# Performance work log

Measured on AMD Instinct MI355X. Metric: run time of the kernel, lower is better.

Reference implementation:

```python
import jax, jax.numpy as jnp
import numpy as np

D_MODEL = 1024
N_HEAD = 16
D_K = D_MODEL // N_HEAD
FFN = 4096
EPS = 1e-5


def layer_norm(x, g, b):
    mu = jnp.mean(x, axis=-1, keepdims=True)
    var = jnp.var(x, axis=-1, keepdims=True)
    return (x - mu) * jax.lax.rsqrt(var + EPS) * g + b


def setup_inputs() -> dict:
    key = jax.random.key(0)
    ks = jax.random.split(key, 16)
    B, L = 2, 2048
    s = 1.0 / np.sqrt(D_MODEL)
    inp = {
        "x": jax.random.normal(ks[0], (B, L, D_MODEL), dtype=jnp.float32),
        "mask": jnp.ones((B, 1, 1, L), dtype=jnp.int32),
        "ln1_g": jnp.ones((D_MODEL,), jnp.float32),
        "ln1_b": jnp.zeros((D_MODEL,), jnp.float32),
        "Wq": jax.random.normal(ks[1], (D_MODEL, D_MODEL), jnp.float32) * s,
        "bq": jnp.zeros((D_MODEL,), jnp.float32),
        "Wk": jax.random.normal(ks[2], (D_MODEL, D_MODEL), jnp.float32) * s,
        "bk": jnp.zeros((D_MODEL,), jnp.float32),
        "Wv": jax.random.normal(ks[3], (D_MODEL, D_MODEL), jnp.float32) * s,
        "bv": jnp.zeros((D_MODEL,), jnp.float32),
        "Wo": jax.random.normal(ks[4], (D_MODEL, D_MODEL), jnp.float32) * s,
        "bo": jnp.zeros((D_MODEL,), jnp.float32),
        "ln2_g": jnp.ones((D_MODEL,), jnp.float32),
        "ln2_b": jnp.zeros((D_MODEL,), jnp.float32),
        "W1": jax.random.normal(ks[5], (D_MODEL, FFN), jnp.float32) * s,
        "b1": jnp.zeros((FFN,), jnp.float32),
        "W2": jax.random.normal(ks[6], (FFN, D_MODEL), jnp.float32) * (1.0 / np.sqrt(FFN)),
        "b2": jnp.zeros((D_MODEL,), jnp.float32),
    }
    return inp


def reference(x, mask, ln1_g, ln1_b, Wq, bq, Wk, bk, Wv, bv, Wo, bo,
              ln2_g, ln2_b, W1, b1, W2, b2):
    B, L, _ = x.shape
    nx = layer_norm(x, ln1_g, ln1_b)
    # QKV projections, split heads -> [B, H, L, Dk]
    def proj(W, b):
        return (nx @ W + b).reshape(B, L, N_HEAD, D_K).transpose(0, 2, 1, 3)
    q, k, v = proj(Wq, bq), proj(Wk, bk), proj(Wv, bv)
    scores = jnp.einsum('bhqd,bhkd->bhqk', q, k) / np.sqrt(D_K)
    scores = jnp.where(mask.astype(bool), scores, -jnp.inf)
    attn = jax.nn.softmax(scores, axis=-1)
    out = jnp.einsum('bhqk,bhkd->bhqd', attn, v)
    out = out.transpose(0, 2, 1, 3).reshape(B, L, D_MODEL)
    out = out @ Wo + bo
    x = x + out  # residual (dropout p=0)
    nx = layer_norm(x, ln2_g, ln2_b)
    h = jax.nn.silu(nx @ W1 + b1)
    x = x + (h @ W2 + b2)
    return x
```

## Files before the change

kernel.cpp:

```cpp
#include <hip/hip_runtime.h>
#include <hip/hip_bf16.h>

#define D_MODEL 1024
#define N_HEAD  16
#define D_K     64
#define FFN_DIM 4096
#define B_SZ    2
#define L_SEQ   2048
#define ROWS    (B_SZ * L_SEQ)
#define PST     68

typedef float  floatx4 __attribute__((ext_vector_type(4)));
typedef short  shortx8 __attribute__((ext_vector_type(8)));

__device__ __forceinline__ unsigned short f2bf(float f) {
    unsigned int u = __float_as_uint(f);
    unsigned int rounding = 0x7fffu + ((u >> 16) & 1u);
    return (unsigned short)((u + rounding) >> 16);
}
__device__ __forceinline__ float bf2f(unsigned short u) {
    return __uint_as_float(((unsigned int)u) << 16);
}

__device__ __forceinline__ void glds16(const unsigned short* g, unsigned short* l) {
    __builtin_amdgcn_global_load_lds(
        (const __attribute__((address_space(1))) unsigned int*)g,
        (__attribute__((address_space(3))) unsigned int*)l, 16, 0, 0);
}

__device__ __forceinline__ void xcd_remap_gemm(int& bx, int& by, int& bz) {
    const int gx = gridDim.x, gy = gridDim.y, gz = gridDim.z;
    const int o = blockIdx.x + gx * (blockIdx.y + gy * blockIdx.z);
    const int nwg = gx * gy * gz;
    const int t = (o & 7) * (nwg >> 3) + (o >> 3);
    const int zsz = gx * gy;
    bz = t / zsz;
    const int w = t - bz * zsz;
    const int grp = w / (8 * gy);
    const int in  = w - grp * (8 * gy);
    by = in >> 3;
    bx = grp * 8 + (in & 7);
}

__global__ __launch_bounds__(256) void ln_kernel(const float* __restrict__ x,
                                                 const float* __restrict__ g,
                                                 const float* __restrict__ b,
                                                 unsigned short* __restrict__ out) {
    const int row = blockIdx.x;
    const int tid = threadIdx.x;
    const float* xr = x + (size_t)row * D_MODEL;
    float4 xv = *reinterpret_cast<const float4*>(&xr[tid * 4]);
    float v[4] = {xv.x, xv.y, xv.z, xv.w};
    float s = v[0] + v[1] + v[2] + v[3];
    float ss = v[0] * v[0] + v[1] * v[1] + v[2] * v[2] + v[3] * v[3];
    __shared__ float r1[256], r2[256];
    r1[tid] = s; r2[tid] = ss;
    __syncthreads();
    for (int off = 128; off > 0; off >>= 1) {
        if (tid < off) { r1[tid] += r1[tid + off]; r2[tid] += r2[tid + off]; }
        __syncthreads();
    }
    const float mean = r1[0] * (1.0f / D_MODEL);
    const float var  = r2[0] * (1.0f / D_MODEL) - mean * mean;
    const float inv  = rsqrtf(var + 1e-5f);
    unsigned short* orow = out + (size_t)row * D_MODEL;
    ushort4 o;
    o.x = f2bf((v[0] - mean) * inv * g[tid * 4 + 0] + b[tid * 4 + 0]);
    o.y = f2bf((v[1] - mean) * inv * g[tid * 4 + 1] + b[tid * 4 + 1]);
    o.z = f2bf((v[2] - mean) * inv * g[tid * 4 + 2] + b[tid * 4 + 2]);
    o.w = f2bf((v[3] - mean) * inv * g[tid * 4 + 3] + b[tid * 4 + 3]);
    *reinterpret_cast<ushort4*>(&orow[tid * 4]) = o;
}

__global__ __launch_bounds__(256) void transpose_cast(const float* __restrict__ W,
                                                      unsigned short* __restrict__ Wt,
                                                      int K, int N) {
    __shared__ unsigned short T[32][33];
    const int t = threadIdx.x;
    const int k0 = blockIdx.y * 32, n0 = blockIdx.x * 32;
    const int kr = t >> 3, nc = (t & 7) * 4;
    float4 w = *reinterpret_cast<const float4*>(&W[(size_t)(k0 + kr) * N + n0 + nc]);
    T[kr][nc + 0] = f2bf(w.x); T[kr][nc + 1] = f2bf(w.y);
    T[kr][nc + 2] = f2bf(w.z); T[kr][nc + 3] = f2bf(w.w);
    __syncthreads();
    const int nr = t >> 3, kc = (t & 7) * 4;
    ushort4 o;
    o.x = T[kc + 0][nr]; o.y = T[kc + 1][nr];
    o.z = T[kc + 2][nr]; o.w = T[kc + 3][nr];
    *reinterpret_cast<ushort4*>(&Wt[(size_t)(n0 + nr) * K + k0 + kc]) = o;
}

__global__ __launch_bounds__(256) void transpose_cast4(const float* s0, const float* s1,
                                                       const float* s2, const float* s3,
                                                       unsigned short* d0, unsigned short* d1,
                                                       unsigned short* d2, unsigned short* d3) {
    const int z = blockIdx.z;
    const float* W = (z == 0) ? s0 : (z == 1) ? s1 : (z == 2) ? s2 : s3;
    unsigned short* Wt = (z == 0) ? d0 : (z == 1) ? d1 : (z == 2) ? d2 : d3;
    __shared__ unsigned short T[32][33];
    const int t = threadIdx.x;
    const int k0 = blockIdx.y * 32, n0 = blockIdx.x * 32;
    const int kr = t >> 3, nc = (t & 7) * 4;
    float4 w = *reinterpret_cast<const float4*>(&W[(size_t)(k0 + kr) * D_MODEL + n0 + nc]);
    T[kr][nc + 0] = f2bf(w.x); T[kr][nc + 1] = f2bf(w.y);
    T[kr][nc + 2] = f2bf(w.z); T[kr][nc + 3] = f2bf(w.w);
    __syncthreads();
    const int nr = t >> 3, kc = (t & 7) * 4;
    ushort4 o;
    o.x = T[kc + 0][nr]; o.y = T[kc + 1][nr];
    o.z = T[kc + 2][nr]; o.w = T[kc + 3][nr];
    *reinterpret_cast<ushort4*>(&Wt[(size_t)(n0 + nr) * D_MODEL + k0 + kc]) = o;
}


template <int SILU, int HAS_RES, int OUT_BF16>
__global__ __launch_bounds__(256) void mfma_gemm(const unsigned short* __restrict__ A,
                                                 const unsigned short* __restrict__ Wt,
                                                 const float* __restrict__ bias,
                                                 const float* __restrict__ res,
                                                 void* __restrict__ outP,
                                                 int M, int N, int K) {
    __shared__ unsigned short As[128 * 32];
    __shared__ unsigned short Bs[128 * 32];
    const int tid  = threadIdx.x;
    const int lane = tid & 63;
    const int wave = tid >> 6;
    int bx, by, bz;
    xcd_remap_gemm(bx, by, bz);
    const int row0 = by * 128, col0 = bx * 128;
    const int wr = (wave >> 1) * 64, wc = (wave & 1) * 64;

    floatx4 acc[4][4] = {};
    const int p0 = tid,       r0s = p0 >> 2, k0s = (((p0 & 3) - (r0s >> 1)) & 3) * 8;
    const int p1 = tid + 256, r1s = p1 >> 2, k1s = (((p1 & 3) - (r1s >> 1)) & 3) * 8;
    const int am = (lane & 15);

    int offA[4], offB[4];
#pragma unroll
    for (int i = 0; i < 4; ++i) {
        const int Ra = wr + i * 16 + am;
        offA[i] = Ra * 32 + (((lane >> 4) + (Ra >> 1)) & 3) * 8;
        const int Rb = wc + i * 16 + am;
        offB[i] = Rb * 32 + (((lane >> 4) + (Rb >> 1)) & 3) * 8;
    }

    for (int kt = 0; kt < K; kt += 32) {
        glds16(A  + (size_t)(row0 + r0s) * K + kt + k0s, &As[p0 * 8]);
        glds16(A  + (size_t)(row0 + r1s) * K + kt + k1s, &As[p1 * 8]);
        glds16(Wt + (size_t)(col0 + r0s) * K + kt + k0s, &Bs[p0 * 8]);
        glds16(Wt + (size_t)(col0 + r1s) * K + kt + k1s, &Bs[p1 * 8]);
        __syncthreads();
        shortx8 af[4], bf[4];
#pragma unroll
        for (int i = 0; i < 4; ++i)
            af[i] = *reinterpret_cast<const shortx8*>(&As[offA[i]]);
#pragma unroll
        for (int j = 0; j < 4; ++j)
            bf[j] = *reinterpret_cast<const shortx8*>(&Bs[offB[j]]);
#pragma unroll
        for (int i = 0; i < 4; ++i)
#pragma unroll
            for (int j = 0; j < 4; ++j)
                acc[i][j] = __builtin_amdgcn_mfma_f32_16x16x32_bf16(af[i], bf[j], acc[i][j], 0, 0, 0);
        __syncthreads();
    }

    const int cq = (lane >> 4) * 4;
    const int cn = lane & 15;
#pragma unroll
    for (int i = 0; i < 4; ++i) {
#pragma unroll
        for (int j = 0; j < 4; ++j) {
            const int n = col0 + wc + j * 16 + cn;
            const float bb = bias[n];
#pragma unroll
            for (int r = 0; r < 4; ++r) {
                const int m = row0 + wr + i * 16 + cq + r;
                float v = acc[i][j][r] + bb;
                if (SILU) v = v / (1.0f + __expf(-v));
                if (HAS_RES) v += res[(size_t)m * N + n];
                if (OUT_BF16) ((unsigned short*)outP)[(size_t)m * N + n] = f2bf(v);
                else          ((float*)outP)[(size_t)m * N + n] = v;
            }
        }
    }
}

__global__ __launch_bounds__(256) void mfma_gemm_qkv(const unsigned short* __restrict__ A,
                                                     const unsigned short* __restrict__ Wt,
                                                     const float* __restrict__ bq,
                                                     const float* __restrict__ bk,
                                                     const float* __restrict__ bv,
                                                     unsigned short* __restrict__ qb,
                                                     unsigned short* __restrict__ kb,
                                                     unsigned short* __restrict__ vtb) {
    const int K = D_MODEL, M = ROWS;
    __shared__ unsigned short As[128 * 32];
    __shared__ unsigned short Bs[128 * 32];
    const int tid  = threadIdx.x;
    const int lane = tid & 63;
    const int wave = tid >> 6;
    int bx, by, bz;
    xcd_remap_gemm(bx, by, bz);
    const int row0 = by * 128, col0 = bx * 128;
    const int wr = (wave >> 1) * 64, wc = (wave & 1) * 64;

    floatx4 acc[4][4] = {};
    const int p0 = tid,       r0s = p0 >> 2, k0s = (((p0 & 3) - (r0s >> 1)) & 3) * 8;
    const int p1 = tid + 256, r1s = p1 >> 2, k1s = (((p1 & 3) - (r1s >> 1)) & 3) * 8;
    const int am = (lane & 15);

    int offA[4], offB[4];
#pragma unroll
    for (int i = 0; i < 4; ++i) {
        const int Ra = wr + i * 16 + am;
        offA[i] = Ra * 32 + (((lane >> 4) + (Ra >> 1)) & 3) * 8;
        const int Rb = wc + i * 16 + am;
        offB[i] = Rb * 32 + (((lane >> 4) + (Rb >> 1)) & 3) * 8;
    }

    for (int kt = 0; kt < K; kt += 32) {
        glds16(A  + (size_t)(row0 + r0s) * K + kt + k0s, &As[p0 * 8]);
        glds16(A  + (size_t)(row0 + r1s) * K + kt + k1s, &As[p1 * 8]);
        glds16(Wt + (size_t)(col0 + r0s) * K + kt + k0s, &Bs[p0 * 8]);
        glds16(Wt + (size_t)(col0 + r1s) * K + kt + k1s, &Bs[p1 * 8]);
        __syncthreads();
        shortx8 af[4], bf[4];
#pragma unroll
        for (int i = 0; i < 4; ++i)
            af[i] = *reinterpret_cast<const shortx8*>(&As[offA[i]]);
#pragma unroll
        for (int j = 0; j < 4; ++j)
            bf[j] = *reinterpret_cast<const shortx8*>(&Bs[offB[j]]);
#pragma unroll
        for (int i = 0; i < 4; ++i)
#pragma unroll
            for (int j = 0; j < 4; ++j)
                acc[i][j] = __builtin_amdgcn_mfma_f32_16x16x32_bf16(af[i], bf[j], acc[i][j], 0, 0, 0);
        __syncthreads();
    }

    const int cq = (lane >> 4) * 4;
    const int cn = lane & 15;
    const int sel = col0 >> 10;
    const int nbase = col0 & 1023;
    const float* bias = (sel == 0) ? bq : (sel == 1) ? bk : bv;
    const float scl = (sel == 0) ? 0.18033688511157292f : 1.0f;
#pragma unroll
    for (int i = 0; i < 4; ++i) {
#pragma unroll
        for (int j = 0; j < 4; ++j) {
            const int n = nbase + wc + j * 16 + cn;
            const float bb = bias[n];
            if (sel == 2) {
                const int m0 = row0 + wr + i * 16 + cq;
                ushort4 o;
                o.x = f2bf(acc[i][j][0] + bb);
                o.y = f2bf(acc[i][j][1] + bb);
                o.z = f2bf(acc[i][j][2] + bb);
                o.w = f2bf(acc[i][j][3] + bb);
                *reinterpret_cast<ushort4*>(&vtb[(size_t)n * M + m0]) = o;
            } else {
                unsigned short* dst = (sel == 0) ? qb : kb;
#pragma unroll
                for (int r = 0; r < 4; ++r) {
                    const int m = row0 + wr + i * 16 + cq + r;
                    dst[(size_t)m * D_MODEL + n] = f2bf((acc[i][j][r] + bb) * scl);
                }
            }
        }
    }
}

__global__ __launch_bounds__(256) void mfma_gemm_splitk(const unsigned short* __restrict__ A,
                                                        const unsigned short* __restrict__ Wt,
                                                        unsigned short* __restrict__ parts,
                                                        int M, int N, int KS) {
    __shared__ unsigned short As[128 * 32];
    __shared__ unsigned short Bs[128 * 32];
    const int tid  = threadIdx.x;
    const int lane = tid & 63;
    const int wave = tid >> 6;
    int bx, by, bz;
    xcd_remap_gemm(bx, by, bz);
    const int row0 = by * 128, col0 = bx * 128;
    const int wr = (wave >> 1) * 64, wc = (wave & 1) * 64;
    const int K = KS * gridDim.z;
    const int kbeg = bz * KS;
    unsigned short* outp = parts + (size_t)bz * M * N;

    floatx4 acc[4][4] = {};
    const int p0 = tid,       r0s = p0 >> 2, k0s = (((p0 & 3) - (r0s >> 1)) & 3) * 8;
    const int p1 = tid + 256, r1s = p1 >> 2, k1s = (((p1 & 3) - (r1s >> 1)) & 3) * 8;
    const int am = (lane & 15);

    int offA[4], offB[4];
#pragma unroll
    for (int i = 0; i < 4; ++i) {
        const int Ra = wr + i * 16 + am;
        offA[i] = Ra * 32 + (((lane >> 4) + (Ra >> 1)) & 3) * 8;
        const int Rb = wc + i * 16 + am;
        offB[i] = Rb * 32 + (((lane >> 4) + (Rb >> 1)) & 3) * 8;
    }

    for (int kt = kbeg; kt < kbeg + KS; kt += 32) {
        glds16(A  + (size_t)(row0 + r0s) * K + kt + k0s, &As[p0 * 8]);
        glds16(A  + (size_t)(row0 + r1s) * K + kt + k1s, &As[p1 * 8]);
        glds16(Wt + (size_t)(col0 + r0s) * K + kt + k0s, &Bs[p0 * 8]);
        glds16(Wt + (size_t)(col0 + r1s) * K + kt + k1s, &Bs[p1 * 8]);
        __syncthreads();
        shortx8 af[4], bf[4];
#pragma unroll
        for (int i = 0; i < 4; ++i)
            af[i] = *reinterpret_cast<const shortx8*>(&As[offA[i]]);
#pragma unroll
        for (int j = 0; j < 4; ++j)
            bf[j] = *reinterpret_cast<const shortx8*>(&Bs[offB[j]]);
#pragma unroll
        for (int i = 0; i < 4; ++i)
#pragma unroll
            for (int j = 0; j < 4; ++j)
                acc[i][j] = __builtin_amdgcn_mfma_f32_16x16x32_bf16(af[i], bf[j], acc[i][j], 0, 0, 0);
        __syncthreads();
    }

    const int cq = (lane >> 4) * 4;
    const int cn = lane & 15;
#pragma unroll
    for (int i = 0; i < 4; ++i)
#pragma unroll
        for (int j = 0; j < 4; ++j) {
            const int n = col0 + wc + j * 16 + cn;
#pragma unroll
            for (int r = 0; r < 4; ++r) {
                const int m = row0 + wr + i * 16 + cq + r;
                outp[(size_t)m * N + n] = f2bf(acc[i][j][r]);
            }
        }
}

__global__ __launch_bounds__(256) void combine_kernel(const unsigned short* __restrict__ p0,
                                                      const unsigned short* __restrict__ p1,
                                                      const float* __restrict__ bias,
                                                      const float* __restrict__ res,
                                                      float* __restrict__ out) {
    const size_t e0 = ((size_t)blockIdx.x * 256 + threadIdx.x) * 4;
    const int col = (int)(e0 & 1023);
    ushort4 a = *reinterpret_cast<const ushort4*>(&p0[e0]);
    ushort4 b = *reinterpret_cast<const ushort4*>(&p1[e0]);
    float4 r = *reinterpret_cast<const float4*>(&res[e0]);
    float4 o;
    o.x = bf2f(a.x) + bf2f(b.x) + bias[col + 0] + r.x;
    o.y = bf2f(a.y) + bf2f(b.y) + bias[col + 1] + r.y;
    o.z = bf2f(a.z) + bf2f(b.z) + bias[col + 2] + r.z;
    o.w = bf2f(a.w) + bf2f(b.w) + bias[col + 3] + r.w;
    *reinterpret_cast<float4*>(&out[e0]) = o;
}

__global__ __launch_bounds__(512) void attn_mfma(const unsigned short* __restrict__ Q,
                                                 const unsigned short* __restrict__ K,
                                                 const unsigned short* __restrict__ Vt,
                                                 const int* __restrict__ mask,
                                                 unsigned short* __restrict__ att) {
    const int tid  = threadIdx.x;
    const int lane = tid & 63;
    const int wave = tid >> 6;
    const int o = blockIdx.x + gridDim.x * (blockIdx.y + gridDim.y * blockIdx.z);
    const int nwg = gridDim.x * gridDim.y * gridDim.z;
    const int t = (o & 7) * (nwg >> 3) + (o >> 3);
    const int qx = t % gridDim.x;
    const int h  = (t / gridDim.x) % gridDim.y;
    const int b  = t / (gridDim.x * gridDim.y);
    const int q0 = qx * 128;

    __shared__ unsigned short Qs[128 * PST];
    __shared__ unsigned short Ks[64 * 64];
    __shared__ unsigned short Vs[64 * 64];
    __shared__ unsigned short Ps[128 * PST];
    __shared__ int mk[64];

    const int am = lane & 15;
    const int aq = (lane >> 4) * 8;
    const int cq = (lane >> 4) * 4;
    const int cn = lane & 15;

    for (int c = tid; c < 1024; c += 512) {
        const int r = c >> 3, off = (c & 7) * 8;
        *reinterpret_cast<uint4*>(&Qs[r * PST + off]) =
            *reinterpret_cast<const uint4*>(&Q[(size_t)(b * L_SEQ + q0 + r) * D_MODEL + h * D_K + off]);
    }

    const int p0 = tid, sr0 = p0 >> 3, sc0 = (((p0 & 7) - sr0) & 7) * 8;
    const unsigned short* K0 = K + (size_t)(b * L_SEQ + sr0) * D_MODEL + h * D_K + sc0;
    const unsigned short* V0 = Vt + (size_t)(h * D_K + sr0) * ROWS + b * L_SEQ + sc0;

    int offF[2][4];
#pragma unroll
    for (int kt = 0; kt < 2; ++kt)
#pragma unroll
        for (int tt = 0; tt < 4; ++tt) {
            const int R = tt * 16 + am;
            offF[kt][tt] = R * 64 + (((kt * 4 + (lane >> 4)) + R) & 7) * 8;
        }

    __syncthreads();

    shortx8 aQ[2];
    aQ[0] = *reinterpret_cast<const shortx8*>(&Qs[(wave * 16 + am) * PST + aq]);
    aQ[1] = *reinterpret_cast<const shortx8*>(&Qs[(wave * 16 + am) * PST + 32 + aq]);

    floatx4 oacc[4] = {};
    float lsum[4] = {0.0f, 0.0f, 0.0f, 0.0f};

    for (int j0 = 0; j0 < L_SEQ; j0 += 64) {
        __syncthreads();
        glds16(K0 + (size_t)j0 * D_MODEL, &Ks[p0 * 8]);
        glds16(V0 + j0, &Vs[p0 * 8]);
        if (tid < 64) mk[tid] = mask[b * L_SEQ + j0 + tid];
        __syncthreads();

        floatx4 sacc[4] = {};
#pragma unroll
        for (int kt = 0; kt < 2; ++kt)
#pragma unroll
            for (int jt = 0; jt < 4; ++jt) {
                shortx8 bK = *reinterpret_cast<const shortx8*>(&Ks[offF[kt][jt]]);
                sacc[jt] = __builtin_amdgcn_mfma_f32_16x16x32_bf16(aQ[kt], bK, sacc[jt], 0, 0, 0);
            }
#pragma unroll
        for (int jt = 0; jt < 4; ++jt) {
            const int mv = mk[jt * 16 + cn];
#pragma unroll
            for (int r = 0; r < 4; ++r) {
                float p = mv ? __builtin_amdgcn_exp2f(sacc[jt][r]) : 0.0f;
                lsum[r] += p;
                Ps[(wave * 16 + cq + r) * PST + jt * 16 + cn] =
                    (unsigned short)(__float_as_uint(p) >> 16);
            }
        }
#pragma unroll
        for (int kt = 0; kt < 2; ++kt) {
            shortx8 aP = *reinterpret_cast<const shortx8*>(&Ps[(wave * 16 + am) * PST + kt * 32 + aq]);
#pragma unroll
            for (int dt = 0; dt < 4; ++dt) {
                shortx8 bV = *reinterpret_cast<const shortx8*>(&Vs[offF[kt][dt]]);
                oacc[dt] = __builtin_amdgcn_mfma_f32_16x16x32_bf16(aP, bV, oacc[dt], 0, 0, 0);
            }
        }
    }

#pragma unroll
    for (int r = 0; r < 4; ++r) {
        float t2 = lsum[r];
        t2 += __shfl_xor(t2, 1);
        t2 += __shfl_xor(t2, 2);
        t2 += __shfl_xor(t2, 4);
        t2 += __shfl_xor(t2, 8);
        lsum[r] = 1.0f / t2;
    }
#pragma unroll
    for (int dt = 0; dt < 4; ++dt)
#pragma unroll
        for (int r = 0; r < 4; ++r) {
            att[(size_t)(b * L_SEQ + q0 + wave * 16 + cq + r) * D_MODEL + h * D_K + dt * 16 + cn] =
                f2bf(oacc[dt][r] * lsum[r]);
        }
}

extern "C" void kernel_launch(void* const* d_in, const int* in_sizes, int n_in,
                              void* d_out, int out_size, void* d_ws, size_t ws_size,
                              hipStream_t stream) {
    const float* x     = (const float*)d_in[0];
    const int*   mask  = (const int*)d_in[1];
    const float* ln1_g = (const float*)d_in[2];
    const float* ln1_b = (const float*)d_in[3];
    const float* Wq    = (const float*)d_in[4];
    const float* bq    = (const float*)d_in[5];
    const float* Wk    = (const float*)d_in[6];
    const float* bk    = (const float*)d_in[7];
    const float* Wv    = (const float*)d_in[8];
    const float* bv    = (const float*)d_in[9];
    const float* Wo    = (const float*)d_in[10];
    const float* bo    = (const float*)d_in[11];
    const float* ln2_g = (const float*)d_in[12];
    const float* ln2_b = (const float*)d_in[13];
    const float* W1    = (const float*)d_in[14];
    const float* b1    = (const float*)d_in[15];
    const float* W2    = (const float*)d_in[16];
    const float* b2    = (const float*)d_in[17];
    float* out = (float*)d_out;

    float* ws = (float*)d_ws;
    const size_t SZ = (size_t)ROWS * D_MODEL;

    unsigned short* nx  = (unsigned short*)(ws + 0 * SZ);
    unsigned short* qb  = (unsigned short*)(ws + 1 * SZ);
    unsigned short* kb  = qb + SZ;
    unsigned short* vtb = (unsigned short*)(ws + 2 * SZ);
    unsigned short* attb = vtb + SZ;
    float* x1  = out;
    unsigned short* nx2 = nx;
    unsigned short* h = (unsigned short*)(ws + 2 * SZ);
    unsigned short* parts = (unsigned short*)(ws + 0 * SZ);

    unsigned short* WqkvT = (unsigned short*)(ws + 4 * SZ);
    unsigned short* WqT = WqkvT;
    unsigned short* WkT = WqkvT + (size_t)D_MODEL * D_MODEL;
    unsigned short* WvT = WkT + (size_t)D_MODEL * D_MODEL;
    unsigned short* WoT = WvT + (size_t)D_MODEL * D_MODEL;
    unsigned short* W1T = (unsigned short*)(ws + 1 * SZ);
    unsigned short* W2T = W1T + (size_t)D_MODEL * FFN_DIM;

    ln_kernel<<<ROWS, 256, 0, stream>>>(x, ln1_g, ln1_b, nx);

    transpose_cast4<<<dim3(32, 32, 4), 256, 0, stream>>>(Wq, Wk, Wv, Wo, WqT, WkT, WvT, WoT);

    mfma_gemm_qkv<<<dim3(3072 / 128, ROWS / 128), 256, 0, stream>>>(
        nx, WqkvT, bq, bk, bv, qb, kb, vtb);

    attn_mfma<<<dim3(L_SEQ / 128, N_HEAD, B_SZ), 512, 0, stream>>>(qb, kb, vtb, mask, attb);

    transpose_cast<<<dim3(FFN_DIM / 32, D_MODEL / 32), 256, 0, stream>>>(W1, W1T, D_MODEL, FFN_DIM);
    transpose_cast<<<dim3(D_MODEL / 32, FFN_DIM / 32), 256, 0, stream>>>(W2, W2T, FFN_DIM, D_MODEL);

    mfma_gemm<0, 1, 0><<<dim3(D_MODEL / 128, ROWS / 128), 256, 0, stream>>>(
        attb, WoT, bo, x, x1, ROWS, D_MODEL, D_MODEL);

    ln_kernel<<<ROWS, 256, 0, stream>>>(x1, ln2_g, ln2_b, nx2);

    mfma_gemm<1, 0, 1><<<dim3(FFN_DIM / 128, ROWS / 128), 256, 0, stream>>>(
        nx2, W1T, b1, nullptr, h, ROWS, FFN_DIM, D_MODEL);

    mfma_gemm_splitk<<<dim3(D_MODEL / 128, ROWS / 128, 2), 256, 0, stream>>>(
        h, W2T, parts, ROWS, D_MODEL, FFN_DIM / 2);
    combine_kernel<<<(ROWS * D_MODEL) / 1024, 256, 0, stream>>>(
        parts, parts + SZ, b2, x1, out);
}
```

Baseline: 393.6 us.

## Double-buffer GEMM LDS tiles and process two K/V chunks per attention sync

All three MFMA GEMM kernels now use ping-pong LDS buffers, so the next 32-wide K slice is issued via global-to-LDS loads while the current slice is computed. This halves the barriers per K step and overlaps load latency with MFMA work. The attention kernel loads two 64-key K/V chunks per iteration, which halves its barrier count. LDS use roughly doubles in the GEMMs and grows in attention, which may lower occupancy. Reusing the shared P buffer across the two inner chunks relies on per-wave row ownership.

After: 366.3 us. -6.9%, faster.

```diff
diff --git a/kernel.cpp b/kernel.cpp
--- a/kernel.cpp
+++ b/kernel.cpp
@@ -113,6 +113,55 @@
 }
 
 
+#define GEMM_STAGE(AS, BS, KT)                                            \
+    do {                                                                  \
+        glds16(A  + sA0 + (KT), &AS[p0 * 8]);                             \
+        glds16(A  + sA1 + (KT), &AS[p1 * 8]);                             \
+        glds16(Wt + sB0 + (KT), &BS[p0 * 8]);                             \
+        glds16(Wt + sB1 + (KT), &BS[p1 * 8]);                             \
+    } while (0)
+
+#define GEMM_COMPUTE(AS, BS)                                              \
+    do {                                                                  \
+        shortx8 af[4], bf[4];                                             \
+        _Pragma("unroll")                                                 \
+        for (int i = 0; i < 4; ++i)                                       \
+            af[i] = *reinterpret_cast<const shortx8*>(&AS[offA[i]]);      \
+        _Pragma("unroll")                                                 \
+        for (int j = 0; j < 4; ++j)                                       \
+            bf[j] = *reinterpret_cast<const shortx8*>(&BS[offB[j]]);      \
+        _Pragma("unroll")                                                 \
+        for (int i = 0; i < 4; ++i)                                       \
+            _Pragma("unroll")                                             \
+            for (int j = 0; j < 4; ++j)                                   \
+                acc[i][j] = __builtin_amdgcn_mfma_f32_16x16x32_bf16(af[i], bf[j], acc[i][j], 0, 0, 0); \
+    } while (0)
+
+#define GEMM_PREAMBLE                                                     \
+    const int tid  = threadIdx.x;                                         \
+    const int lane = tid & 63;                                            \
+    const int wave = tid >> 6;                                            \
+    int bx, by, bz;                                                       \
+    xcd_remap_gemm(bx, by, bz);                                           \
+    const int row0 = by * 128, col0 = bx * 128;                           \
+    const int wr = (wave >> 1) * 64, wc = (wave & 1) * 64;                \
+    floatx4 acc[4][4] = {};                                               \
+    const int p0 = tid,       r0s = p0 >> 2, k0s = (((p0 & 3) - (r0s >> 1)) & 3) * 8; \
+    const int p1 = tid + 256, r1s = p1 >> 2, k1s = (((p1 & 3) - (r1s >> 1)) & 3) * 8; \
+    const int am = (lane & 15);                                           \
+    const size_t sA0 = (size_t)(row0 + r0s) * K + k0s;                    \
+    const size_t sA1 = (size_t)(row0 + r1s) * K + k1s;                    \
+    const size_t sB0 = (size_t)(col0 + r0s) * K + k0s;                    \
+    const size_t sB1 = (size_t)(col0 + r1s) * K + k1s;                    \
+    int offA[4], offB[4];                                                 \
+    _Pragma("unroll")                                                     \
+    for (int i = 0; i < 4; ++i) {                                         \
+        const int Ra = wr + i * 16 + am;                                  \
+        offA[i] = Ra * 32 + (((lane >> 4) + (Ra >> 1)) & 3) * 8;          \
+        const int Rb = wc + i * 16 + am;                                  \
+        offB[i] = Rb * 32 + (((lane >> 4) + (Rb >> 1)) & 3) * 8;          \
+    }
+
 template <int SILU, int HAS_RES, int OUT_BF16>
 __global__ __launch_bounds__(256) void mfma_gemm(const unsigned short* __restrict__ A,
                                                  const unsigned short* __restrict__ Wt,
@@ -120,48 +169,18 @@
                                                  const float* __restrict__ res,
                                                  void* __restrict__ outP,
                                                  int M, int N, int K) {
-    __shared__ unsigned short As[128 * 32];
-    __shared__ unsigned short Bs[128 * 32];
-    const int tid  = threadIdx.x;
-    const int lane = tid & 63;
-    const int wave = tid >> 6;
-    int bx, by, bz;
-    xcd_remap_gemm(bx, by, bz);
-    const int row0 = by * 128, col0 = bx * 128;
-    const int wr = (wave >> 1) * 64, wc = (wave & 1) * 64;
-
-    floatx4 acc[4][4] = {};
-    const int p0 = tid,       r0s = p0 >> 2, k0s = (((p0 & 3) - (r0s >> 1)) & 3) * 8;
-    const int p1 = tid + 256, r1s = p1 >> 2, k1s = (((p1 & 3) - (r1s >> 1)) & 3) * 8;
-    const int am = (lane & 15);
-
-    int offA[4], offB[4];
-#pragma unroll
-    for (int i = 0; i < 4; ++i) {
-        const int Ra = wr + i * 16 + am;
-        offA[i] = Ra * 32 + (((lane >> 4) + (Ra >> 1)) & 3) * 8;
-        const int Rb = wc + i * 16 + am;
-        offB[i] = Rb * 32 + (((lane >> 4) + (Rb >> 1)) & 3) * 8;
-    }
-
-    for (int kt = 0; kt < K; kt += 32) {
-        glds16(A  + (size_t)(row0 + r0s) * K + kt + k0s, &As[p0 * 8]);
-        glds16(A  + (size_t)(row0 + r1s) * K + kt + k1s, &As[p1 * 8]);
-        glds16(Wt + (size_t)(col0 + r0s) * K + kt + k0s, &Bs[p0 * 8]);
-        glds16(Wt + (size_t)(col0 + r1s) * K + kt + k1s, &Bs[p1 * 8]);
-        __syncthreads();
-        shortx8 af[4], bf[4];
-#pragma unroll
-        for (int i = 0; i < 4; ++i)
-            af[i] = *reinterpret_cast<const shortx8*>(&As[offA[i]]);
-#pragma unroll
-        for (int j = 0; j < 4; ++j)
-            bf[j] = *reinterpret_cast<const shortx8*>(&Bs[offB[j]]);
-#pragma unroll
-        for (int i = 0; i < 4; ++i)
-#pragma unroll
-            for (int j = 0; j < 4; ++j)
-                acc[i][j] = __builtin_amdgcn_mfma_f32_16x16x32_bf16(af[i], bf[j], acc[i][j], 0, 0, 0);
+    __shared__ unsigned short As0[128 * 32], As1[128 * 32];
+    __shared__ unsigned short Bs0[128 * 32], Bs1[128 * 32];
+    GEMM_PREAMBLE
+
+    GEMM_STAGE(As0, Bs0, 0);
+    __syncthreads();
+    for (int kt = 0; kt < K; kt += 64) {
+        GEMM_STAGE(As1, Bs1, kt + 32);
+        GEMM_COMPUTE(As0, Bs0);
+        __syncthreads();
+        if (kt + 64 < K) GEMM_STAGE(As0, Bs0, kt + 64);
+        GEMM_COMPUTE(As1, Bs1);
         __syncthreads();
     }
 
@@ -195,48 +214,18 @@
                                                      unsigned short* __restrict__ kb,
                                                      unsigned short* __restrict__ vtb) {
     const int K = D_MODEL, M = ROWS;
-    __shared__ unsigned short As[128 * 32];
-    __shared__ unsigned short Bs[128 * 32];
-    const int tid  = threadIdx.x;
-    const int lane = tid & 63;
-    const int wave = tid >> 6;
-    int bx, by, bz;
-    xcd_remap_gemm(bx, by, bz);
-    const int row0 = by * 128, col0 = bx * 128;
-    const int wr = (wave >> 1) * 64, wc = (wave & 1) * 64;
-
-    floatx4 acc[4][4] = {};
-    const int p0 = tid,       r0s = p0 >> 2, k0s = (((p0 & 3) - (r0s >> 1)) & 3) * 8;
-    const int p1 = tid + 256, r1s = p1 >> 2, k1s = (((p1 & 3) - (r1s >> 1)) & 3) * 8;
-    const int am = (lane & 15);
-
-    int offA[4], offB[4];
-#pragma unroll
-    for (int i = 0; i < 4; ++i) {
-        const int Ra = wr + i * 16 + am;
-        offA[i] = Ra * 32 + (((lane >> 4) + (Ra >> 1)) & 3) * 8;
-        const int Rb = wc + i * 16 + am;
-        offB[i] = Rb * 32 + (((lane >> 4) + (Rb >> 1)) & 3) * 8;
-    }
-
-    for (int kt = 0; kt < K; kt += 32) {
-        glds16(A  + (size_t)(row0 + r0s) * K + kt + k0s, &As[p0 * 8]);
-        glds16(A  + (size_t)(row0 + r1s) * K + kt + k1s, &As[p1 * 8]);
-        glds16(Wt + (size_t)(col0 + r0s) * K + kt + k0s, &Bs[p0 * 8]);
-        glds16(Wt + (size_t)(col0 + r1s) * K + kt + k1s, &Bs[p1 * 8]);
-        __syncthreads();
-        shortx8 af[4], bf[4];
-#pragma unroll
-        for (int i = 0; i < 4; ++i)
-            af[i] = *reinterpret_cast<const shortx8*>(&As[offA[i]]);
-#pragma unroll
-        for (int j = 0; j < 4; ++j)
-            bf[j] = *reinterpret_cast<const shortx8*>(&Bs[offB[j]]);
-#pragma unroll
-        for (int i = 0; i < 4; ++i)
-#pragma unroll
-            for (int j = 0; j < 4; ++j)
-                acc[i][j] = __builtin_amdgcn_mfma_f32_16x16x32_bf16(af[i], bf[j], acc[i][j], 0, 0, 0);
+    __shared__ unsigned short As0[128 * 32], As1[128 * 32];
+    __shared__ unsigned short Bs0[128 * 32], Bs1[128 * 32];
+    GEMM_PREAMBLE
+
+    GEMM_STAGE(As0, Bs0, 0);
+    __syncthreads();
+    for (int kt = 0; kt < K; kt += 64) {
+        GEMM_STAGE(As1, Bs1, kt + 32);
+        GEMM_COMPUTE(As0, Bs0);
+        __syncthreads();
+        if (kt + 64 < K) GEMM_STAGE(As0, Bs0, kt + 64);
+        GEMM_COMPUTE(As1, Bs1);
         __syncthreads();
     }
 
@@ -276,51 +265,21 @@
                                                         const unsigned short* __restrict__ Wt,
                                                         unsigned short* __restrict__ parts,
                                                         int M, int N, int KS) {
-    __shared__ unsigned short As[128 * 32];
-    __shared__ unsigned short Bs[128 * 32];
-    const int tid  = threadIdx.x;
-    const int lane = tid & 63;
-    const int wave = tid >> 6;
-    int bx, by, bz;
-    xcd_remap_gemm(bx, by, bz);
-    const int row0 = by * 128, col0 = bx * 128;
-    const int wr = (wave >> 1) * 64, wc = (wave & 1) * 64;
+    __shared__ unsigned short As0[128 * 32], As1[128 * 32];
+    __shared__ unsigned short Bs0[128 * 32], Bs1[128 * 32];
     const int K = KS * gridDim.z;
+    GEMM_PREAMBLE
     const int kbeg = bz * KS;
     unsigned short* outp = parts + (size_t)bz * M * N;
 
-    floatx4 acc[4][4] = {};
-    const int p0 = tid,       r0s = p0 >> 2, k0s = (((p0 & 3) - (r0s >> 1)) & 3) * 8;
-    const int p1 = tid + 256, r1s = p1 >> 2, k1s = (((p1 & 3) - (r1s >> 1)) & 3) * 8;
-    const int am = (lane & 15);
-
-    int offA[4], offB[4];
-#pragma unroll
-    for (int i = 0; i < 4; ++i) {
-        const int Ra = wr + i * 16 + am;
-        offA[i] = Ra * 32 + (((lane >> 4) + (Ra >> 1)) & 3) * 8;
-        const int Rb = wc + i * 16 + am;
-        offB[i] = Rb * 32 + (((lane >> 4) + (Rb >> 1)) & 3) * 8;
-    }
-
-    for (int kt = kbeg; kt < kbeg + KS; kt += 32) {
-        glds16(A  + (size_t)(row0 + r0s) * K + kt + k0s, &As[p0 * 8]);
-        glds16(A  + (size_t)(row0 + r1s) * K + kt + k1s, &As[p1 * 8]);
-        glds16(Wt + (size_t)(col0 + r0s) * K + kt + k0s, &Bs[p0 * 8]);
-        glds16(Wt + (size_t)(col0 + r1s) * K + kt + k1s, &Bs[p1 * 8]);
-        __syncthreads();
-        shortx8 af[4], bf[4];
-#pragma unroll
-        for (int i = 0; i < 4; ++i)
-            af[i] = *reinterpret_cast<const shortx8*>(&As[offA[i]]);
-#pragma unroll
-        for (int j = 0; j < 4; ++j)
-            bf[j] = *reinterpret_cast<const shortx8*>(&Bs[offB[j]]);
-#pragma unroll
-        for (int i = 0; i < 4; ++i)
-#pragma unroll
-            for (int j = 0; j < 4; ++j)
-                acc[i][j] = __builtin_amdgcn_mfma_f32_16x16x32_bf16(af[i], bf[j], acc[i][j], 0, 0, 0);
+    GEMM_STAGE(As0, Bs0, kbeg);
+    __syncthreads();
+    for (int kt = kbeg; kt < kbeg + KS; kt += 64) {
+        GEMM_STAGE(As1, Bs1, kt + 32);
+        GEMM_COMPUTE(As0, Bs0);
+        __syncthreads();
+        if (kt + 64 < kbeg + KS) GEMM_STAGE(As0, Bs0, kt + 64);
+        GEMM_COMPUTE(As1, Bs1);
         __syncthreads();
     }
 
@@ -374,10 +333,10 @@
     const int q0 = qx * 128;
 
     __shared__ unsigned short Qs[128 * PST];
-    __shared__ unsigned short Ks[64 * 64];
-    __shared__ unsigned short Vs[64 * 64];
+    __shared__ unsigned short Ks[2][64 * 64];
+    __shared__ unsigned short Vs[2][64 * 64];
     __shared__ unsigned short Ps[128 * PST];
-    __shared__ int mk[64];
+    __shared__ int mk[128];
 
     const int am = lane & 15;
     const int aq = (lane >> 4) * 8;
@@ -412,39 +371,44 @@
     floatx4 oacc[4] = {};
     float lsum[4] = {0.0f, 0.0f, 0.0f, 0.0f};
 
-    for (int j0 = 0; j0 < L_SEQ; j0 += 64) {
-        __syncthreads();
-        glds16(K0 + (size_t)j0 * D_MODEL, &Ks[p0 * 8]);
-        glds16(V0 + j0, &Vs[p0 * 8]);
-        if (tid < 64) mk[tid] = mask[b * L_SEQ + j0 + tid];
-        __syncthreads();
-
-        floatx4 sacc[4] = {};
-#pragma unroll
-        for (int kt = 0; kt < 2; ++kt)
+    for (int j0 = 0; j0 < L_SEQ; j0 += 128) {
+        __syncthreads();
+        glds16(K0 + (size_t)j0 * D_MODEL,        &Ks[0][p0 * 8]);
+        glds16(K0 + (size_t)(j0 + 64) * D_MODEL, &Ks[1][p0 * 8]);
+        glds16(V0 + j0,      &Vs[0][p0 * 8]);
+        glds16(V0 + j0 + 64, &Vs[1][p0 * 8]);
+        if (tid < 128) mk[tid] = mask[b * L_SEQ + j0 + tid];
+        __syncthreads();
+
+#pragma unroll
+        for (int u = 0; u < 2; ++u) {
+            floatx4 sacc[4] = {};
+#pragma unroll
+            for (int kt = 0; kt < 2; ++kt)
+#pragma unroll
+                for (int jt = 0; jt < 4; ++jt) {
+                    shortx8 bK = *reinterpret_cast<const shortx8*>(&Ks[u][offF[kt][jt]]);
+                    sacc[jt] = __builtin_amdgcn_mfma_f32_16x16x32_bf16(aQ[kt], bK, sacc[jt], 0, 0, 0);
+                }
 #pragma unroll
             for (int jt = 0; jt < 4; ++jt) {
-                shortx8 bK = *reinterpret_cast<const shortx8*>(&Ks[offF[kt][jt]]);
-                sacc[jt] = __builtin_amdgcn_mfma_f32_16x16x32_bf16(aQ[kt], bK, sacc[jt], 0, 0, 0);
+                const int mv = mk[u * 64 + jt * 16 + cn];
+#pragma unroll
+                for (int r = 0; r < 4; ++r) {
+                    float p = mv ? __builtin_amdgcn_exp2f(sacc[jt][r]) : 0.0f;
+                    lsum[r] += p;
+                    Ps[(wave * 16 + cq + r) * PST + jt * 16 + cn] =
+                        (unsigned short)(__float_as_uint(p) >> 16);
+                }
             }
 #pragma unroll
-        for (int jt = 0; jt < 4; ++jt) {
-            const int mv = mk[jt * 16 + cn];
-#pragma unroll
-            for (int r = 0; r < 4; ++r) {
-                float p = mv ? __builtin_amdgcn_exp2f(sacc[jt][r]) : 0.0f;
-                lsum[r] += p;
-                Ps[(wave * 16 + cq + r) * PST + jt * 16 + cn] =
-                    (unsigned short)(__float_as_uint(p) >> 16);
-            }
-        }
-#pragma unroll
-        for (int kt = 0; kt < 2; ++kt) {
-            shortx8 aP = *reinterpret_cast<const shortx8*>(&Ps[(wave * 16 + am) * PST + kt * 32 + aq]);
-#pragma unroll
-            for (int dt = 0; dt < 4; ++dt) {
-                shortx8 bV = *reinterpret_cast<const shortx8*>(&Vs[offF[kt][dt]]);
-                oacc[dt] = __builtin_amdgcn_mfma_f32_16x16x32_bf16(aP, bV, oacc[dt], 0, 0, 0);
+            for (int kt = 0; kt < 2; ++kt) {
+                shortx8 aP = *reinterpret_cast<const shortx8*>(&Ps[(wave * 16 + am) * PST + kt * 32 + aq]);
+#pragma unroll
+                for (int dt = 0; dt < 4; ++dt) {
+                    shortx8 bV = *reinterpret_cast<const shortx8*>(&Vs[u][offF[kt][dt]]);
+                    oacc[dt] = __builtin_amdgcn_mfma_f32_16x16x32_bf16(aP, bV, oacc[dt], 0, 0, 0);
+                }
             }
         }
     }
```
